# Kernel optimization log

Hardware: AMD Instinct MI355X
Metric: run time of the kernel (lower is better)

The kernel has to match this reference:

```python
import jax, jax.numpy as jnp
import numpy as np

E = 1152          # embed_dim (Qwen3-VL vision hidden_size)
H = 16            # num_heads
D = E // H        # head_dim = 72
SEG = 8           # number of frames / attention segments
HW = 32           # each frame is 32x32 patches -> seg_len = 1024
L = HW * HW
S = SEG * L       # total tokens = 8192


def _make_rotary(S):
    # VisionRotaryEmbedding(dim=head_dim//2): inv_freq over arange(0, 36, 2)/36 -> 18 freqs
    half = D // 2  # 36
    inv_freq = 1.0 / (10000.0 ** (jnp.arange(0, half, 2, dtype=jnp.float32) / half))  # (18,)
    # 2D (h,w) position ids within each 32x32 frame, tiled across frames
    hpos = jnp.tile(jnp.repeat(jnp.arange(HW, dtype=jnp.float32), HW), SEG)  # (S,)
    wpos = jnp.tile(jnp.tile(jnp.arange(HW, dtype=jnp.float32), HW), SEG)    # (S,)
    fh = hpos[:, None] * inv_freq[None, :]   # (S, 18)
    fw = wpos[:, None] * inv_freq[None, :]   # (S, 18)
    freqs = jnp.concatenate([fh, fw], axis=-1)       # (S, 36)
    emb = jnp.concatenate([freqs, freqs], axis=-1)   # (S, 72) = head_dim
    return jnp.cos(emb), jnp.sin(emb)


def setup_inputs() -> dict:
    key = jax.random.key(0)
    k = jax.random.split(key, 6)
    std = 1.0 / np.sqrt(E)
    cos, sin = _make_rotary(S)
    return {
        "x": jax.random.normal(k[0], (S, E), jnp.float32),
        "cos": cos,
        "sin": sin,
        "qkv_w": jax.random.normal(k[1], (3 * E, E), jnp.float32) * std,
        "qkv_b": jax.random.normal(k[2], (3 * E,), jnp.float32) * 0.02,
        "proj_w": jax.random.normal(k[3], (E, E), jnp.float32) * std,
        "proj_b": jax.random.normal(k[4], (E,), jnp.float32) * 0.02,
        "cu_seqlens": jnp.arange(SEG + 1, dtype=jnp.int32) * L,
    }


def _rope(t, cos, sin):
    # t: (S, H, D); cos/sin: (S, D) broadcast over heads (matches cos.unsqueeze(1))
    half = t.shape[-1] // 2
    t1, t2 = t[..., :half], t[..., half:]
    rot = jnp.concatenate([-t2, t1], axis=-1)
    return t * cos[:, None, :] + rot * sin[:, None, :]


def reference(x, cos, sin, qkv_w, qkv_b, proj_w, proj_b, cu_seqlens):
    S_, E_ = x.shape
    qkv = x @ qkv_w.T + qkv_b                     # (S, 3E)
    q, k, v = jnp.split(qkv, 3, axis=-1)
    q = _rope(q.reshape(S_, H, D), cos, sin)
    k = _rope(k.reshape(S_, H, D), cos, sin)
    v = v.reshape(S_, H, D)
    # Equal-length segments (one per frame): block-diagonal attention via reshape,
    # honoring cu_seqlens structure without materializing an (S, S) mask.
    nseg = cu_seqlens.shape[0] - 1
    Lseg = S_ // nseg
    qs = q.reshape(nseg, Lseg, H, D)
    ks = k.reshape(nseg, Lseg, H, D)
    vs = v.reshape(nseg, Lseg, H, D)
    scale = 1.0 / np.sqrt(D)
    logits = jnp.einsum('gqhd,gkhd->ghqk', qs, ks) * scale   # (nseg, H, L, L)
    attn = jax.nn.softmax(logits, axis=-1)
    out = jnp.einsum('ghqk,gkhd->gqhd', attn, vs).reshape(S_, E_)
    return out @ proj_w.T + proj_b
```

## Files before the change

### kernel.cpp

```cpp
#include <hip/hip_runtime.h>
#include <hip/hip_bf16.h>
#include <stdint.h>

#define SEGN 8
#define LSEG 1024
#define SS   8192
#define EE   1152
#define HH   16
#define DD   72
#define DP   96
#define E3   3456
#define E3P  3584
#define EEP  1280

typedef __attribute__((ext_vector_type(8)))  __bf16 bf16x8;
typedef __attribute__((ext_vector_type(4)))  float  f32x4;
typedef __attribute__((ext_vector_type(16))) float  f32x16;
typedef __attribute__((ext_vector_type(4)))  unsigned int u32x4;

__device__ __forceinline__ short f2b(float x) {
  __hip_bfloat16 h = __float2bfloat16(x);
  return __builtin_bit_cast(short, h);
}
__device__ __forceinline__ float b2f(short x) {
  return __bfloat162float(__builtin_bit_cast(__hip_bfloat16, x));
}
__device__ __forceinline__ unsigned int pk2(float x, float y) {
  return (unsigned int)(unsigned short)f2b(x) |
         ((unsigned int)(unsigned short)f2b(y) << 16);
}
__device__ __forceinline__ void gload16(const void* g, void* l) {
  __builtin_amdgcn_global_load_lds(
      (const __attribute__((address_space(1))) unsigned int*)g,
      (__attribute__((address_space(3))) unsigned int*)l, 16, 0, 0);
}

#define BAR() __builtin_amdgcn_s_barrier()
#define LGKM0() do { asm volatile("s_waitcnt lgkmcnt(0)" ::: "memory"); \
                     __builtin_amdgcn_sched_barrier(0); } while (0)

__global__ void k_cvt(const float* __restrict__ in, short* __restrict__ out, int n4) {
  int i = blockIdx.x * blockDim.x + threadIdx.x;
  int stride = gridDim.x * blockDim.x;
  for (; i < n4; i += stride) {
    float4 v = reinterpret_cast<const float4*>(in)[i];
    short4 o;
    o.x = f2b(v.x); o.y = f2b(v.y); o.z = f2b(v.z); o.w = f2b(v.w);
    reinterpret_cast<short4*>(out)[i] = o;
  }
}

template <int OUT_BF16>
__global__ __launch_bounds__(512, 2) void k_gemm256(
    const short* __restrict__ A, const short* __restrict__ B,
    const float* __restrict__ bias, void* __restrict__ Cout,
    int K, int Nreal)
{
  __shared__ __align__(16) short Als[2][4][64 * 64];
  __shared__ __align__(16) short Bls[2][4][64 * 64];
  const int t = threadIdx.x;
  const int lane = t & 63, wave = t >> 6;
  const int r16 = lane & 15, kg = lane >> 4;
  const int wm = wave >> 2, wn = wave & 3;

  const int nwg = gridDim.x * gridDim.y;
  const int fid = blockIdx.y * gridDim.x + blockIdx.x;
  const int cpx = nwg >> 3;
  const int swz = (fid & 7) * cpx + (fid >> 3);
  const int m0 = (swz % gridDim.x) * 256, n0 = (swz / gridDim.x) * 256;
  const int NT = K >> 6;

  const int D = t * 16;
  const int L = D ^ (((D >> 7) & 7) << 4);
  const int srow = L >> 7, scol = (L & 127) >> 1;
  const short* pa = A + (size_t)(m0 + srow) * K + scol;
  const short* pb = B + (size_t)(n0 + srow) * K + scol;
  const int K64 = K * 64;

#define STAGE_A(bf, h, kt_) do { \
    gload16(pa + (h) * K64 + (kt_) * 64, (char*)Als[bf][h] + D); \
    gload16(pa + ((h) + 2) * K64 + (kt_) * 64, (char*)Als[bf][(h) + 2] + D); } while (0)
#define STAGE_B(bf, h, kt_) do { \
    gload16(pb + (h) * K64 + (kt_) * 64, (char*)Bls[bf][h] + D); \
    gload16(pb + ((h) + 2) * K64 + (kt_) * 64, (char*)Bls[bf][(h) + 2] + D); } while (0)

  const int cA0 = (kg * 16) ^ ((r16 & 7) << 4);
  const int cA1 = (64 + kg * 16) ^ ((r16 & 7) << 4);

  f32x4 acc[8][4] = {};

  STAGE_A(0, 0, 0); STAGE_B(0, 0, 0);
  STAGE_A(0, 1, 0); STAGE_B(0, 1, 0);
  STAGE_A(1, 0, 1); STAGE_B(1, 0, 1);
  asm volatile("s_waitcnt vmcnt(4)" ::: "memory");
  BAR();

  for (int kt = 0; kt < NT; ++kt) {
    const int bsel = kt & 1, bn1 = bsel ^ 1;
    const bool s1 = (kt + 1 < NT), s2 = (kt + 2 < NT);
    const char* aq0 = (const char*)Als[bsel][2 * wm];
    const char* aq1 = (const char*)Als[bsel][2 * wm + 1];
    const char* bq  = (const char*)Bls[bsel][wn];

    bf16x8 a_[2][2], b_[4][2];

#pragma unroll
    for (int mi = 0; mi < 2; ++mi) {
      a_[mi][0] = *(const bf16x8*)(aq0 + (mi * 16 + r16) * 128 + cA0);
      a_[mi][1] = *(const bf16x8*)(aq0 + (mi * 16 + r16) * 128 + cA1);
    }
#pragma unroll
    for (int n = 0; n < 4; ++n) {
      b_[n][0] = *(const bf16x8*)(bq + (n * 16 + r16) * 128 + cA0);
      b_[n][1] = *(const bf16x8*)(bq + (n * 16 + r16) * 128 + cA1);
    }
    if (s1) STAGE_A(bn1, 1, kt + 1);
    BAR();
    LGKM0();
    __builtin_amdgcn_s_setprio(1);
#pragma unroll
    for (int mi = 0; mi < 2; ++mi)
#pragma unroll
      for (int n = 0; n < 4; ++n) {
        acc[mi][n] = __builtin_amdgcn_mfma_f32_16x16x32_bf16(a_[mi][0], b_[n][0], acc[mi][n], 0, 0, 0);
        acc[mi][n] = __builtin_amdgcn_mfma_f32_16x16x32_bf16(a_[mi][1], b_[n][1], acc[mi][n], 0, 0, 0);
      }
    __builtin_amdgcn_s_setprio(0);
    BAR();

#pragma unroll
    for (int mi = 0; mi < 2; ++mi) {
      a_[mi][0] = *(const bf16x8*)(aq0 + ((mi + 2) * 16 + r16) * 128 + cA0);
      a_[mi][1] = *(const bf16x8*)(aq0 + ((mi + 2) * 16 + r16) * 128 + cA1);
    }
    if (s1) STAGE_B(bn1, 1, kt + 1);
    BAR();
    LGKM0();
    __builtin_amdgcn_s_setprio(1);
#pragma unroll
    for (int mi = 0; mi < 2; ++mi)
#pragma unroll
      for (int n = 0; n < 4; ++n) {
        acc[mi + 2][n] = __builtin_amdgcn_mfma_f32_16x16x32_bf16(a_[mi][0], b_[n][0], acc[mi + 2][n], 0, 0, 0);
        acc[mi + 2][n] = __builtin_amdgcn_mfma_f32_16x16x32_bf16(a_[mi][1], b_[n][1], acc[mi + 2][n], 0, 0, 0);
      }
    __builtin_amdgcn_s_setprio(0);
    BAR();

#pragma unroll
    for (int mi = 0; mi < 2; ++mi) {
      a_[mi][0] = *(const bf16x8*)(aq1 + (mi * 16 + r16) * 128 + cA0);
      a_[mi][1] = *(const bf16x8*)(aq1 + (mi * 16 + r16) * 128 + cA1);
    }
    if (s2) STAGE_A(bsel, 0, kt + 2);
    BAR();
    LGKM0();
    __builtin_amdgcn_s_setprio(1);
#pragma unroll
    for (int mi = 0; mi < 2; ++mi)
#pragma unroll
      for (int n = 0; n < 4; ++n) {
        acc[mi + 4][n] = __builtin_amdgcn_mfma_f32_16x16x32_bf16(a_[mi][0], b_[n][0], acc[mi + 4][n], 0, 0, 0);
        acc[mi + 4][n] = __builtin_amdgcn_mfma_f32_16x16x32_bf16(a_[mi][1], b_[n][1], acc[mi + 4][n], 0, 0, 0);
      }
    __builtin_amdgcn_s_setprio(0);
    BAR();

#pragma unroll
    for (int mi = 0; mi < 2; ++mi) {
      a_[mi][0] = *(const bf16x8*)(aq1 + ((mi + 2) * 16 + r16) * 128 + cA0);
      a_[mi][1] = *(const bf16x8*)(aq1 + ((mi + 2) * 16 + r16) * 128 + cA1);
    }
    if (s2) STAGE_B(bsel, 0, kt + 2);
    BAR();
    LGKM0();
    __builtin_amdgcn_s_setprio(1);
#pragma unroll
    for (int mi = 0; mi < 2; ++mi)
#pragma unroll
      for (int n = 0; n < 4; ++n) {
        acc[mi + 6][n] = __builtin_amdgcn_mfma_f32_16x16x32_bf16(a_[mi][0], b_[n][0], acc[mi + 6][n], 0, 0, 0);
        acc[mi + 6][n] = __builtin_amdgcn_mfma_f32_16x16x32_bf16(a_[mi][1], b_[n][1], acc[mi + 6][n], 0, 0, 0);
      }
    __builtin_amdgcn_s_setprio(0);
    if (s2) { asm volatile("s_waitcnt vmcnt(4)" ::: "memory"); }
    else    { asm volatile("s_waitcnt vmcnt(0)" ::: "memory"); }
    BAR();
  }
#undef STAGE_A
#undef STAGE_B

#pragma unroll
  for (int n = 0; n < 4; ++n) {
    int col = n0 + wn * 64 + n * 16 + r16;
    if (col < Nreal) {
      float bv = bias[col];
#pragma unroll
      for (int m = 0; m < 8; ++m)
#pragma unroll
        for (int r = 0; r < 4; ++r) {
          int row = m0 + wm * 128 + m * 16 + kg * 4 + r;
          float v = acc[m][n][r] + bv;
          if (OUT_BF16) ((short*)Cout)[(size_t)row * Nreal + col] = f2b(v);
          else          ((float*)Cout)[(size_t)row * Nreal + col] = v;
        }
    }
  }
}

__global__ __launch_bounds__(256) void k_rope(
    const short* __restrict__ qkv, const float* __restrict__ cosb, const float* __restrict__ sinb,
    short* __restrict__ Qg, short* __restrict__ Kg, short* __restrict__ Vg)
{
  __shared__ short vt[72][64];
  const int b = blockIdx.x;
  const int seg = b >> 8, head = (b >> 4) & 15, pb = b & 15;
  const int pos0 = pb * 64;
  const int t = threadIdx.x;
  const int sh = seg * 16 + head;
  const float qscale = 0.17002540410995343f;

#pragma unroll
  for (int i = 0; i < 24; ++i) {
    int e = t + i * 256;
    int p = e / 96, d = e % 96;
    int s = seg * 1024 + pos0 + p;
    int ob = (sh * 1024 + pos0 + p) * 96 + d;
    short qo = 0, ko = 0;
    if (d < 72) {
      int base = s * E3 + head * 72;
      float c = cosb[s * 72 + d], sn = sinb[s * 72 + d];
      int d2 = d < 36 ? d + 36 : d - 36;
      float sgn = d < 36 ? -1.f : 1.f;
      float q1 = b2f(qkv[base + d]),        q2 = b2f(qkv[base + d2]);
      float k1 = b2f(qkv[base + 1152 + d]), k2 = b2f(qkv[base + 1152 + d2]);
      qo = f2b((q1 * c + sgn * q2 * sn) * qscale);
      ko = f2b(k1 * c + sgn * k2 * sn);
    }
    Qg[ob] = qo;
    Kg[ob] = ko;
  }
  for (int i = 0; i < 18; ++i) {
    int e = t + i * 256;
    int p = e / 72, d = e % 72;
    int s = seg * 1024 + pos0 + p;
    vt[d][p] = qkv[s * E3 + 2304 + head * 72 + d];
  }
  __syncthreads();
#pragma unroll
  for (int i = 0; i < 24; ++i) {
    int e = t + i * 256;
    int d = e >> 6, p = e & 63;
    short v;
    if (d < 72)       v = vt[d][p];
    else if (d == 72) v = (short)0x3F80;
    else              v = 0;
    Vg[(sh * 96 + d) * 1024 + pos0 + p] = v;
  }
}

#define KSS 104
#define VTS 72
__global__ __launch_bounds__(256, 3) void k_attn(
    const short* __restrict__ Qg, const short* __restrict__ Kg, const short* __restrict__ Vg,
    short* __restrict__ Og)
{
  __shared__ __align__(16) short Ks[64 * KSS];
  __shared__ __align__(16) short VT[96 * VTS];
  const int p_ = blockIdx.x;
  const int xcd = p_ & 7, rest = p_ >> 3;
  const int qb = rest & 7, shi = rest >> 3;
  const int sh = xcd * 16 + shi;
  const int seg = sh >> 4, head = sh & 15;
  const int t = threadIdx.x, lane = t & 63, wave = t >> 6;
  const int l31 = lane & 31, hi = lane >> 5;
  const int q0 = qb * 128 + wave * 32;

  bf16x8 qf[6];
  {
    const short* qp = Qg + ((size_t)(sh * 1024 + q0 + l31)) * 96 + hi * 8;
#pragma unroll
    for (int dm = 0; dm < 6; ++dm) qf[dm] = *(const bf16x8*)(qp + dm * 16);
  }

  const short* kbase = Kg + (size_t)sh * 1024 * 96;
  const short* vbase = Vg + (size_t)sh * 96 * 1024;
  int koff[4], voff[4];
#pragma unroll
  for (int i = 0; i < 4; ++i) {
    int c = t + i * 256;
    int kr = c / 13, kc8 = c - kr * 13;
    koff[i] = kr * 96 + ((kc8 == 12) ? 0 : kc8 * 8);
    int vr = c / 9, vc8 = c - vr * 9;
    voff[i] = vr * 1024 + ((vc8 == 8) ? 0 : vc8 * 8);
  }

  f32x16 acc0 = {}, acc1 = {}, acc2 = {};
  float Mrun = -1e30f;

  for (int kt = 0; kt < 16; ++kt) {
    __syncthreads();
    {
      const short* kp = kbase + kt * 64 * 96;
      const short* vp = vbase + kt * 64;
#pragma unroll
      for (int i = 0; i < 3; ++i) {
        gload16(kp + koff[i], (char*)Ks + (t + i * 256) * 16);
        gload16(vp + voff[i], (char*)VT + (t + i * 256) * 16);
      }
      if (t < 64) gload16(kp + koff[3], (char*)Ks + (t + 768) * 16);
      if (t < 96) gload16(vp + voff[3], (char*)VT + (t + 768) * 16);
    }
    __syncthreads();

    f32x16 s0 = {}, s1 = {};
#pragma unroll
    for (int dm = 0; dm < 6; ++dm) {
      bf16x8 kf0 = *(const bf16x8*)&Ks[l31 * KSS + dm * 16 + hi * 8];
      bf16x8 kf1 = *(const bf16x8*)&Ks[(32 + l31) * KSS + dm * 16 + hi * 8];
      s0 = __builtin_amdgcn_mfma_f32_32x32x16_bf16(kf0, qf[dm], s0, 0, 0, 0);
      s1 = __builtin_amdgcn_mfma_f32_32x32x16_bf16(kf1, qf[dm], s1, 0, 0, 0);
    }

    float pmax = s0[0];
#pragma unroll
    for (int r = 1; r < 16; ++r) pmax = fmaxf(pmax, s0[r]);
#pragma unroll
    for (int r = 0; r < 16; ++r) pmax = fmaxf(pmax, s1[r]);
    pmax = fmaxf(pmax, __shfl_xor(pmax, 32));

    if (__any(pmax > Mrun + 8.0f)) {
      float mn = fmaxf(Mrun, pmax);
      float corr = exp2f(Mrun - mn);
      Mrun = mn;
#pragma unroll
      for (int r = 0; r < 16; ++r) {
        int qr = (r & 3) + 8 * (r >> 2) + 4 * hi;
        float cr = __shfl(corr, qr);
        acc0[r] *= cr; acc1[r] *= cr; acc2[r] *= cr;
      }
    }

    unsigned int pk0[8], pk1[8];
#pragma unroll
    for (int b = 0; b < 4; ++b)
#pragma unroll
      for (int i = 0; i < 2; ++i) {
        pk0[b * 2 + i] = pk2(exp2f(s0[b * 4 + 2 * i] - Mrun), exp2f(s0[b * 4 + 2 * i + 1] - Mrun));
        pk1[b * 2 + i] = pk2(exp2f(s1[b * 4 + 2 * i] - Mrun), exp2f(s1[b * 4 + 2 * i + 1] - Mrun));
      }

#pragma unroll
    for (int ks = 0; ks < 4; ++ks) {
      const int k1 = ks & 1;
      unsigned int A0, A1, B0, B1;
      if (ks < 2) { A0 = pk0[4 * k1]; A1 = pk0[4 * k1 + 1]; B0 = pk0[4 * k1 + 2]; B1 = pk0[4 * k1 + 3]; }
      else        { A0 = pk1[4 * k1]; A1 = pk1[4 * k1 + 1]; B0 = pk1[4 * k1 + 2]; B1 = pk1[4 * k1 + 3]; }
      unsigned int SA0 = __shfl_xor((int)A0, 32), SA1 = __shfl_xor((int)A1, 32);
      unsigned int SB0 = __shfl_xor((int)B0, 32), SB1 = __shfl_xor((int)B1, 32);
      u32x4 wv;
      wv.x = hi ? SB0 : A0;
      wv.y = hi ? SB1 : A1;
      wv.z = hi ? B0 : SA0;
      wv.w = hi ? B1 : SA1;
      bf16x8 af = __builtin_bit_cast(bf16x8, wv);
      bf16x8 vf0 = *(const bf16x8*)&VT[l31 * VTS + ks * 16 + hi * 8];
      bf16x8 vf1 = *(const bf16x8*)&VT[(32 + l31) * VTS + ks * 16 + hi * 8];
      bf16x8 vf2 = *(const bf16x8*)&VT[(64 + l31) * VTS + ks * 16 + hi * 8];
      acc0 = __builtin_amdgcn_mfma_f32_32x32x16_bf16(af, vf0, acc0, 0, 0, 0);
      acc1 = __builtin_amdgcn_mfma_f32_32x32x16_bf16(af, vf1, acc1, 0, 0, 0);
      acc2 = __builtin_amdgcn_mfma_f32_32x32x16_bf16(af, vf2, acc2, 0, 0, 0);
    }
  }

#pragma unroll
  for (int r = 0; r < 16; ++r) {
    float l = __shfl(acc2[r], (lane & 32) | 8);
    float inv = 1.0f / l;
    int q = q0 + (r & 3) + 8 * (r >> 2) + 4 * hi;
    size_t base = (size_t)(seg * 1024 + q) * 1152 + head * 72;
    Og[base + l31]      = f2b(acc0[r] * inv);
    Og[base + 32 + l31] = f2b(acc1[r] * inv);
    if (l31 < 8) Og[base + 64 + l31] = f2b(acc2[r] * inv);
  }
}

extern "C" void kernel_launch(void* const* d_in, const int* in_sizes, int n_in,
                              void* d_out, int out_size, void* d_ws, size_t ws_size,
                              hipStream_t stream) {
  (void)in_sizes; (void)n_in; (void)out_size; (void)ws_size;
  const float* x      = (const float*)d_in[0];
  const float* cosb   = (const float*)d_in[1];
  const float* sinb   = (const float*)d_in[2];
  const float* qkv_w  = (const float*)d_in[3];
  const float* qkv_b  = (const float*)d_in[4];
  const float* proj_w = (const float*)d_in[5];
  const float* proj_b = (const float*)d_in[6];

  char* ws = (char*)d_ws;
  size_t o = 0;
  short* xb  = (short*)(ws + o); o += (size_t)SS * EE * 2;
  short* qwb = (short*)(ws + o); o += (size_t)E3P * EE * 2;
  short* pwb = (short*)(ws + o); o += (size_t)EEP * EE * 2;
  short* qkv = (short*)(ws + o); o += (size_t)SS * E3 * 2;
  short* Qg  = (short*)(ws + o); o += (size_t)SEGN * HH * LSEG * DP * 2;
  short* Kg  = (short*)(ws + o); o += (size_t)SEGN * HH * LSEG * DP * 2;
  short* Vg  = (short*)(ws + o); o += (size_t)SEGN * HH * DP * LSEG * 2;
  short* og  = xb;

  k_cvt<<<2048, 256, 0, stream>>>(x, xb, SS * EE / 4);
  k_cvt<<<1024, 256, 0, stream>>>(qkv_w, qwb, E3 * EE / 4);
  k_cvt<<<512, 256, 0, stream>>>(proj_w, pwb, EE * EE / 4);

  dim3 g1(SS / 256, E3P / 256);
  k_gemm256<1><<<g1, 512, 0, stream>>>(xb, qwb, qkv_b, qkv, EE, E3);

  k_rope<<<SEGN * HH * 16, 256, 0, stream>>>(qkv, cosb, sinb, Qg, Kg, Vg);

  k_attn<<<SEGN * HH * 8, 256, 0, stream>>>(Qg, Kg, Vg, og);

  dim3 g2(SS / 256, EEP / 256);
  k_gemm256<0><<<g2, 512, 0, stream>>>(og, pwb, proj_b, d_out, EE, EE);
}
```

Baseline: 271.4 us.

## Double-buffer K/V tiles in attention and trim padded QK head-dim work

```diff
diff --git a/kernel.cpp b/kernel.cpp
--- a/kernel.cpp
+++ b/kernel.cpp
@@ -36,8 +36,6 @@
 }
 
 #define BAR() __builtin_amdgcn_s_barrier()
-#define LGKM0() do { asm volatile("s_waitcnt lgkmcnt(0)" ::: "memory"); \
-                     __builtin_amdgcn_sched_barrier(0); } while (0)
 
 __global__ void k_cvt(const float* __restrict__ in, short* __restrict__ out, int n4) {
   int i = blockIdx.x * blockDim.x + threadIdx.x;
@@ -62,12 +60,7 @@
   const int lane = t & 63, wave = t >> 6;
   const int r16 = lane & 15, kg = lane >> 4;
   const int wm = wave >> 2, wn = wave & 3;
-
-  const int nwg = gridDim.x * gridDim.y;
-  const int fid = blockIdx.y * gridDim.x + blockIdx.x;
-  const int cpx = nwg >> 3;
-  const int swz = (fid & 7) * cpx + (fid >> 3);
-  const int m0 = (swz % gridDim.x) * 256, n0 = (swz / gridDim.x) * 256;
+  const int m0 = blockIdx.x * 256, n0 = blockIdx.y * 256;
   const int NT = K >> 6;
 
   const int D = t * 16;
@@ -116,7 +109,6 @@
     }
     if (s1) STAGE_A(bn1, 1, kt + 1);
     BAR();
-    LGKM0();
     __builtin_amdgcn_s_setprio(1);
 #pragma unroll
     for (int mi = 0; mi < 2; ++mi)
@@ -135,7 +127,6 @@
     }
     if (s1) STAGE_B(bn1, 1, kt + 1);
     BAR();
-    LGKM0();
     __builtin_amdgcn_s_setprio(1);
 #pragma unroll
     for (int mi = 0; mi < 2; ++mi)
@@ -154,7 +145,6 @@
     }
     if (s2) STAGE_A(bsel, 0, kt + 2);
     BAR();
-    LGKM0();
     __builtin_amdgcn_s_setprio(1);
 #pragma unroll
     for (int mi = 0; mi < 2; ++mi)
@@ -173,7 +163,6 @@
     }
     if (s2) STAGE_B(bsel, 0, kt + 2);
     BAR();
-    LGKM0();
     __builtin_amdgcn_s_setprio(1);
 #pragma unroll
     for (int mi = 0; mi < 2; ++mi)
@@ -261,12 +250,12 @@
 
 #define KSS 104
 #define VTS 72
-__global__ __launch_bounds__(256, 3) void k_attn(
+__global__ __launch_bounds__(256, 2) void k_attn(
     const short* __restrict__ Qg, const short* __restrict__ Kg, const short* __restrict__ Vg,
     short* __restrict__ Og)
 {
-  __shared__ __align__(16) short Ks[64 * KSS];
-  __shared__ __align__(16) short VT[96 * VTS];
+  __shared__ __align__(16) short Ks[2][64 * KSS];
+  __shared__ __align__(16) short VT[2][96 * VTS];
   const int p_ = blockIdx.x;
   const int xcd = p_ & 7, rest = p_ >> 3;
   const int qb = rest & 7, shi = rest >> 3;
@@ -276,11 +265,11 @@
   const int l31 = lane & 31, hi = lane >> 5;
   const int q0 = qb * 128 + wave * 32;
 
-  bf16x8 qf[6];
+  bf16x8 qf[5];
   {
     const short* qp = Qg + ((size_t)(sh * 1024 + q0 + l31)) * 96 + hi * 8;
 #pragma unroll
-    for (int dm = 0; dm < 6; ++dm) qf[dm] = *(const bf16x8*)(qp + dm * 16);
+    for (int dm = 0; dm < 5; ++dm) qf[dm] = *(const bf16x8*)(qp + dm * 16);
   }
 
   const short* kbase = Kg + (size_t)sh * 1024 * 96;
@@ -298,29 +287,44 @@
   f32x16 acc0 = {}, acc1 = {}, acc2 = {};
   float Mrun = -1e30f;
 
+  {
+    const short* kp = kbase;
+    const short* vp = vbase;
+#pragma unroll
+    for (int i = 0; i < 3; ++i) {
+      gload16(kp + koff[i], (char*)Ks[0] + (t + i * 256) * 16);
+      gload16(vp + voff[i], (char*)VT[0] + (t + i * 256) * 16);
+    }
+    if (t < 64) gload16(kp + koff[3], (char*)Ks[0] + (t + 768) * 16);
+    if (t < 96) gload16(vp + voff[3], (char*)VT[0] + (t + 768) * 16);
+  }
+  __syncthreads();
+
   for (int kt = 0; kt < 16; ++kt) {
-    __syncthreads();
-    {
-      const short* kp = kbase + kt * 64 * 96;
-      const short* vp = vbase + kt * 64;
+    const int cur = kt & 1;
+    if (kt < 15) {
+      const int nb = cur ^ 1;
+      const short* kp = kbase + (kt + 1) * 64 * 96;
+      const short* vp = vbase + (kt + 1) * 64;
 #pragma unroll
       for (int i = 0; i < 3; ++i) {
-        gload16(kp + koff[i], (char*)Ks + (t + i * 256) * 16);
-        gload16(vp + voff[i], (char*)VT + (t + i * 256) * 16);
-      }
-      if (t < 64) gload16(kp + koff[3], (char*)Ks + (t + 768) * 16);
-      if (t < 96) gload16(vp + voff[3], (char*)VT + (t + 768) * 16);
-    }
-    __syncthreads();
+        gload16(kp + koff[i], (char*)Ks[nb] + (t + i * 256) * 16);
+        gload16(vp + voff[i], (char*)VT[nb] + (t + i * 256) * 16);
+      }
+      if (t < 64) gload16(kp + koff[3], (char*)Ks[nb] + (t + 768) * 16);
+      if (t < 96) gload16(vp + voff[3], (char*)VT[nb] + (t + 768) * 16);
+    }
 
     f32x16 s0 = {}, s1 = {};
-#pragma unroll
-    for (int dm = 0; dm < 6; ++dm) {
-      bf16x8 kf0 = *(const bf16x8*)&Ks[l31 * KSS + dm * 16 + hi * 8];
-      bf16x8 kf1 = *(const bf16x8*)&Ks[(32 + l31) * KSS + dm * 16 + hi * 8];
+    __builtin_amdgcn_s_setprio(1);
+#pragma unroll
+    for (int dm = 0; dm < 5; ++dm) {
+      bf16x8 kf0 = *(const bf16x8*)&Ks[cur][l31 * KSS + dm * 16 + hi * 8];
+      bf16x8 kf1 = *(const bf16x8*)&Ks[cur][(32 + l31) * KSS + dm * 16 + hi * 8];
       s0 = __builtin_amdgcn_mfma_f32_32x32x16_bf16(kf0, qf[dm], s0, 0, 0, 0);
       s1 = __builtin_amdgcn_mfma_f32_32x32x16_bf16(kf1, qf[dm], s1, 0, 0, 0);
     }
+    __builtin_amdgcn_s_setprio(0);
 
     float pmax = s0[0];
 #pragma unroll
@@ -350,6 +354,7 @@
         pk1[b * 2 + i] = pk2(exp2f(s1[b * 4 + 2 * i] - Mrun), exp2f(s1[b * 4 + 2 * i + 1] - Mrun));
       }
 
+    __builtin_amdgcn_s_setprio(1);
 #pragma unroll
     for (int ks = 0; ks < 4; ++ks) {
       const int k1 = ks & 1;
@@ -364,13 +369,16 @@
       wv.z = hi ? B0 : SA0;
       wv.w = hi ? B1 : SA1;
       bf16x8 af = __builtin_bit_cast(bf16x8, wv);
-      bf16x8 vf0 = *(const bf16x8*)&VT[l31 * VTS + ks * 16 + hi * 8];
-      bf16x8 vf1 = *(const bf16x8*)&VT[(32 + l31) * VTS + ks * 16 + hi * 8];
-      bf16x8 vf2 = *(const bf16x8*)&VT[(64 + l31) * VTS + ks * 16 + hi * 8];
+      bf16x8 vf0 = *(const bf16x8*)&VT[cur][l31 * VTS + ks * 16 + hi * 8];
+      bf16x8 vf1 = *(const bf16x8*)&VT[cur][(32 + l31) * VTS + ks * 16 + hi * 8];
+      bf16x8 vf2 = *(const bf16x8*)&VT[cur][(64 + l31) * VTS + ks * 16 + hi * 8];
       acc0 = __builtin_amdgcn_mfma_f32_32x32x16_bf16(af, vf0, acc0, 0, 0, 0);
       acc1 = __builtin_amdgcn_mfma_f32_32x32x16_bf16(af, vf1, acc1, 0, 0, 0);
       acc2 = __builtin_amdgcn_mfma_f32_32x32x16_bf16(af, vf2, acc2, 0, 0, 0);
     }
+    __builtin_amdgcn_s_setprio(0);
+
+    __syncthreads();
   }
 
 #pragma unroll
```

New measurement: 264.8 us. 1.02x faster.
